# Optimization experiments

Hardware: AMD Instinct MI355X
Metric: run time of the kernel (lower is better)

## Reference

```python
import jax, jax.numpy as jnp
import numpy as np

HIER_WEIGHT = 0.1

def setup_inputs() -> dict:
    key = jax.random.key(0)
    k1, k2, k3, k4, k5 = jax.random.split(key, 5)
    B, N, D = 128, 100000, 256
    E = N - 1
    return {
        "logits": jax.random.normal(k1, (B, N), dtype=jnp.float32),
        "labels": jax.random.randint(k2, (B,), 0, N, dtype=jnp.int64),
        "label_emb": jax.random.normal(k3, (N, D), dtype=jnp.float32),
        "parent_idx": jax.random.randint(k4, (E,), 0, N, dtype=jnp.int64),
        "child_idx": jax.random.randint(k5, (E,), 0, N, dtype=jnp.int64),
    }

def reference(logits, labels, label_emb, parent_idx, child_idx):
    # base loss: mean cross-entropy over the batch (loss_fn)
    logp = jax.nn.log_softmax(logits, axis=-1)                      # [B, N]
    ce = -jnp.take_along_axis(logp, labels[:, None], axis=-1)       # [B, 1]
    base_loss = jnp.mean(ce)
    # hierarchy penalty: sum over all (parent, child) edges of ||p - c||_2^2
    diff = label_emb[parent_idx] - label_emb[child_idx]             # [E, D]
    recursive_loss = jnp.sum(diff * diff)
    return base_loss + HIER_WEIGHT * recursive_loss
```

## Files before the change

kernel.cpp:

```cpp
#include <hip/hip_runtime.h>
#include <math.h>


#define THREADS    1024
#define WAVES      (THREADS / 64)
#define EDGE_BATCH 16

__global__ __launch_bounds__(THREADS) void hier_fused_kernel(
    const float* __restrict__ logits,
    const int* __restrict__ labels,
    const float* __restrict__ emb,
    const int* __restrict__ parent,
    const int* __restrict__ child,
    float* __restrict__ out,
    int B, int N, int D, int E, int edge_blocks)
{
    __shared__ float red[WAVES];
    const int tid  = threadIdx.x;
    const int lane = tid & 63;
    const int wv   = tid >> 6;
    const float L2E = 1.4426950408889634f;

    if ((int)blockIdx.x < edge_blocks) {
        const int wave = blockIdx.x * WAVES + wv;
        const int base = wave * EDGE_BATCH;
        const int d4   = D >> 2;

        float acc = 0.0f;
        if (base < E) {
            const int n = min(EDGE_BATCH, E - base);
            int idx = 0;
            if (lane < EDGE_BATCH) {
                if (lane < n) idx = parent[base + lane];
            } else if (lane >= 32 && lane < 32 + EDGE_BATCH) {
                const int j = lane - 32;
                if (j < n) idx = child[base + j];
            }
            const float4* __restrict__ emb4 = (const float4*)emb;

            if (d4 == 64) {
                #pragma unroll 4
                for (int j = 0; j < n; ++j) {
                    const int p = __shfl(idx, j);
                    const int c = __shfl(idx, j + 32);
                    float4 a = emb4[(size_t)p * 64 + lane];
                    float4 b = emb4[(size_t)c * 64 + lane];
                    float dx = a.x - b.x, dy = a.y - b.y;
                    float dz = a.z - b.z, dw = a.w - b.w;
                    acc += dx * dx + dy * dy + dz * dz + dw * dw;
                }
            } else {
                for (int j = 0; j < n; ++j) {
                    const int p = __shfl(idx, j);
                    const int c = __shfl(idx, j + 32);
                    for (int d = lane; d < d4; d += 64) {
                        float4 a = emb4[(size_t)p * d4 + d];
                        float4 b = emb4[(size_t)c * d4 + d];
                        float dx = a.x - b.x, dy = a.y - b.y;
                        float dz = a.z - b.z, dw = a.w - b.w;
                        acc += dx * dx + dy * dy + dz * dz + dw * dw;
                    }
                }
            }
        }

        #pragma unroll
        for (int off = 32; off; off >>= 1) acc += __shfl_xor(acc, off);
        if (lane == 0) red[wv] = acc;
        __syncthreads();
        if (tid == 0) {
            float t = 0.0f;
            #pragma unroll
            for (int i = 0; i < WAVES; ++i) t += red[i];
            atomicAdd(out, 0.1f * t);
        }
    } else {
        const int row = (int)blockIdx.x - edge_blocks;
        const float* __restrict__ rp = logits + (size_t)row * (size_t)N;
        const float4* __restrict__ rp4 = (const float4*)rp;
        const int n4 = N >> 2;

        float s = 0.0f;
        for (int i = tid; i < n4; i += THREADS) {
            float4 v = rp4[i];
            s += exp2f(v.x * L2E) + exp2f(v.y * L2E)
               + exp2f(v.z * L2E) + exp2f(v.w * L2E);
        }
        const int rem = N & 3;
        if (tid < rem) s += exp2f(rp[(size_t)(n4 << 2) + tid] * L2E);

        #pragma unroll
        for (int off = 32; off; off >>= 1) s += __shfl_xor(s, off);
        if (lane == 0) red[wv] = s;
        __syncthreads();
        if (tid == 0) {
            float S = 0.0f;
            #pragma unroll
            for (int i = 0; i < WAVES; ++i) S += red[i];
            const int lab = labels[row];
            const float ce = logf(S) - rp[(size_t)lab];
            atomicAdd(out, ce * (1.0f / (float)B));
        }
    }
}

extern "C" void kernel_launch(void* const* d_in, const int* in_sizes, int n_in,
                              void* d_out, int out_size, void* d_ws, size_t ws_size,
                              hipStream_t stream) {
    const float* logits = (const float*)d_in[0];
    const int*   labels = (const int*)d_in[1];
    const float* emb    = (const float*)d_in[2];
    const int*   parent = (const int*)d_in[3];
    const int*   child  = (const int*)d_in[4];
    float* out = (float*)d_out;

    const int B = in_sizes[1];
    const int N = in_sizes[0] / B;
    const int E = in_sizes[3];
    const int D = in_sizes[2] / N;

    const int n_waves     = (E + EDGE_BATCH - 1) / EDGE_BATCH;
    const int edge_blocks = (n_waves + WAVES - 1) / WAVES;

    hipMemsetAsync(d_out, 0, sizeof(float), stream);
    hipLaunchKernelGGL(hier_fused_kernel, dim3(edge_blocks + B), dim3(THREADS),
                       0, stream, logits, labels, emb, parent, child, out,
                       B, N, D, E, edge_blocks);
}
```

Baseline: 50.93 us.

## Reorganize fused kernel: logits rows first, 8-lane-per-edge gather, smaller blocks

Cuts the block size from 1024 to 256 threads and places the 128 logit-row blocks ahead of the edge blocks, so the long-running softmax rows are scheduled first. The logsumexp loop is unrolled 4x with independent accumulators to keep more loads in flight. The edge gather now assigns 8 lanes per edge (8 edges per wave, each lane reading 8 float4s) instead of one edge per wave-iteration after shuffles, which raises memory-level parallelism and removes the serial per-edge loop. The cost is far more blocks, each doing an atomicAdd, so there is more atomic traffic on one address. The edge path now hardcodes D=256 and drops the general-D fallback.

```diff
diff --git a/kernel.cpp b/kernel.cpp
--- a/kernel.cpp
+++ b/kernel.cpp
@@ -2,66 +2,86 @@
 #include <math.h>
 
 
-#define THREADS    1024
-#define WAVES      (THREADS / 64)
-#define EDGE_BATCH 16
+#define TPB 256
+#define WPB (TPB / 64)
+#define EPW 8
 
-__global__ __launch_bounds__(THREADS) void hier_fused_kernel(
+__global__ __launch_bounds__(TPB, 4) void hier_fused_kernel(
     const float* __restrict__ logits,
     const int* __restrict__ labels,
     const float* __restrict__ emb,
     const int* __restrict__ parent,
     const int* __restrict__ child,
     float* __restrict__ out,
-    int B, int N, int D, int E, int edge_blocks)
+    int B, int N, int D, int E)
 {
-    __shared__ float red[WAVES];
+    __shared__ float red[WPB];
     const int tid  = threadIdx.x;
     const int lane = tid & 63;
     const int wv   = tid >> 6;
     const float L2E = 1.4426950408889634f;
 
-    if ((int)blockIdx.x < edge_blocks) {
-        const int wave = blockIdx.x * WAVES + wv;
-        const int base = wave * EDGE_BATCH;
-        const int d4   = D >> 2;
+    if ((int)blockIdx.x < B) {
+        const int row = blockIdx.x;
+        const float* __restrict__ rp = logits + (size_t)row * (size_t)N;
+        const float4* __restrict__ rp4 = (const float4*)rp;
+        const int n4 = N >> 2;
+
+        float s0 = 0.0f, s1 = 0.0f, s2 = 0.0f, s3 = 0.0f;
+        int i = tid;
+        for (; i + 3 * TPB < n4; i += 4 * TPB) {
+            float4 v0 = rp4[i];
+            float4 v1 = rp4[i + TPB];
+            float4 v2 = rp4[i + 2 * TPB];
+            float4 v3 = rp4[i + 3 * TPB];
+            s0 += exp2f(v0.x * L2E) + exp2f(v0.y * L2E)
+                + exp2f(v0.z * L2E) + exp2f(v0.w * L2E);
+            s1 += exp2f(v1.x * L2E) + exp2f(v1.y * L2E)
+                + exp2f(v1.z * L2E) + exp2f(v1.w * L2E);
+            s2 += exp2f(v2.x * L2E) + exp2f(v2.y * L2E)
+                + exp2f(v2.z * L2E) + exp2f(v2.w * L2E);
+            s3 += exp2f(v3.x * L2E) + exp2f(v3.y * L2E)
+                + exp2f(v3.z * L2E) + exp2f(v3.w * L2E);
+        }
+        for (; i < n4; i += TPB) {
+            float4 v = rp4[i];
+            s0 += exp2f(v.x * L2E) + exp2f(v.y * L2E)
+                + exp2f(v.z * L2E) + exp2f(v.w * L2E);
+        }
+        const int rem = N & 3;
+        if (tid < rem) s0 += exp2f(rp[(size_t)(n4 << 2) + tid] * L2E);
+        float s = (s0 + s1) + (s2 + s3);
+
+        #pragma unroll
+        for (int off = 32; off; off >>= 1) s += __shfl_xor(s, off);
+        if (lane == 0) red[wv] = s;
+        __syncthreads();
+        if (tid == 0) {
+            float S = 0.0f;
+            #pragma unroll
+            for (int k = 0; k < WPB; ++k) S += red[k];
+            const int lab = labels[row];
+            atomicAdd(out, (logf(S) - rp[(size_t)lab]) * (1.0f / (float)B));
+        }
+    } else {
+        const int wave = ((int)blockIdx.x - B) * WPB + wv;
+        const int g    = lane >> 3;
+        const int sub  = lane & 7;
+        const int e    = wave * EPW + g;
+
+        int p = 0, c = 0;
+        if (e < E) { p = parent[e]; c = child[e]; }
+        const float4* __restrict__ pr = (const float4*)emb + (size_t)p * 64;
+        const float4* __restrict__ cr = (const float4*)emb + (size_t)c * 64;
 
         float acc = 0.0f;
-        if (base < E) {
-            const int n = min(EDGE_BATCH, E - base);
-            int idx = 0;
-            if (lane < EDGE_BATCH) {
-                if (lane < n) idx = parent[base + lane];
-            } else if (lane >= 32 && lane < 32 + EDGE_BATCH) {
-                const int j = lane - 32;
-                if (j < n) idx = child[base + j];
-            }
-            const float4* __restrict__ emb4 = (const float4*)emb;
-
-            if (d4 == 64) {
-                #pragma unroll 4
-                for (int j = 0; j < n; ++j) {
-                    const int p = __shfl(idx, j);
-                    const int c = __shfl(idx, j + 32);
-                    float4 a = emb4[(size_t)p * 64 + lane];
-                    float4 b = emb4[(size_t)c * 64 + lane];
-                    float dx = a.x - b.x, dy = a.y - b.y;
-                    float dz = a.z - b.z, dw = a.w - b.w;
-                    acc += dx * dx + dy * dy + dz * dz + dw * dw;
-                }
-            } else {
-                for (int j = 0; j < n; ++j) {
-                    const int p = __shfl(idx, j);
-                    const int c = __shfl(idx, j + 32);
-                    for (int d = lane; d < d4; d += 64) {
-                        float4 a = emb4[(size_t)p * d4 + d];
-                        float4 b = emb4[(size_t)c * d4 + d];
-                        float dx = a.x - b.x, dy = a.y - b.y;
-                        float dz = a.z - b.z, dw = a.w - b.w;
-                        acc += dx * dx + dy * dy + dz * dz + dw * dw;
-                    }
-                }
-            }
+        #pragma unroll
+        for (int k = 0; k < 8; ++k) {
+            float4 a = pr[sub + k * 8];
+            float4 b = cr[sub + k * 8];
+            const float dx = a.x - b.x, dy = a.y - b.y;
+            const float dz = a.z - b.z, dw = a.w - b.w;
+            acc += dx * dx + dy * dy + dz * dz + dw * dw;
         }
 
         #pragma unroll
@@ -71,35 +91,8 @@
         if (tid == 0) {
             float t = 0.0f;
             #pragma unroll
-            for (int i = 0; i < WAVES; ++i) t += red[i];
+            for (int k = 0; k < WPB; ++k) t += red[k];
             atomicAdd(out, 0.1f * t);
-        }
-    } else {
-        const int row = (int)blockIdx.x - edge_blocks;
-        const float* __restrict__ rp = logits + (size_t)row * (size_t)N;
-        const float4* __restrict__ rp4 = (const float4*)rp;
-        const int n4 = N >> 2;
-
-        float s = 0.0f;
-        for (int i = tid; i < n4; i += THREADS) {
-            float4 v = rp4[i];
-            s += exp2f(v.x * L2E) + exp2f(v.y * L2E)
-               + exp2f(v.z * L2E) + exp2f(v.w * L2E);
-        }
-        const int rem = N & 3;
-        if (tid < rem) s += exp2f(rp[(size_t)(n4 << 2) + tid] * L2E);
-
-        #pragma unroll
-        for (int off = 32; off; off >>= 1) s += __shfl_xor(s, off);
-        if (lane == 0) red[wv] = s;
-        __syncthreads();
-        if (tid == 0) {
-            float S = 0.0f;
-            #pragma unroll
-            for (int i = 0; i < WAVES; ++i) S += red[i];
-            const int lab = labels[row];
-            const float ce = logf(S) - rp[(size_t)lab];
-            atomicAdd(out, ce * (1.0f / (float)B));
         }
     }
 }
@@ -119,11 +112,11 @@
     const int E = in_sizes[3];
     const int D = in_sizes[2] / N;
 
-    const int n_waves     = (E + EDGE_BATCH - 1) / EDGE_BATCH;
-    const int edge_blocks = (n_waves + WAVES - 1) / WAVES;
+    const int n_edge_waves  = (E + EPW - 1) / EPW;
+    const int n_edge_blocks = (n_edge_waves + WPB - 1) / WPB;
 
     hipMemsetAsync(d_out, 0, sizeof(float), stream);
-    hipLaunchKernelGGL(hier_fused_kernel, dim3(edge_blocks + B), dim3(THREADS),
+    hipLaunchKernelGGL(hier_fused_kernel, dim3(B + n_edge_blocks), dim3(TPB),
                        0, stream, logits, labels, emb, parent, child, out,
-                       B, N, D, E, edge_blocks);
+                       B, N, D, E);
 }
```

Result: slower. 67.99 us (+33.5%).
